# Optimization experiments

Measured on AMD Instinct MI355X. Metric: run time of the kernel, lower is better.

The kernel has to match this reference:

```python
import jax, jax.numpy as jnp
import numpy as np

NBINS = 256
EARLY_STOP = 0.1  # fraction of nbins with no improvement before early break


def setup_inputs() -> dict:
    key = jax.random.key(0)
    x = jax.random.uniform(key, (8, 3, 1024, 1024), dtype=jnp.float32)
    return {"x": x}


def _otsu_forward(x):
    orig_shape = x.shape
    b, c, h, w = x.shape
    rows = b * c
    xf = x.reshape(rows, h * w)                      # (R, N) one image per row
    N = xf.shape[1]

    # Per-row shift so each row starts at 0 (mirrors `x = (x.T - min_value).T`).
    min_val = xf.min(axis=1, keepdims=True)          # (R, 1)
    xs = xf - min_val
    gmax = xs.max()                                  # global min of xs is 0, global max here
    edges = jnp.linspace(jnp.zeros((), xs.dtype), gmax, NBINS + 1)
    width = gmax / NBINS

    # Per-row histogram with torch.histc semantics over global [0, gmax].
    bin_idx = jnp.clip(jnp.floor(xs / width).astype(jnp.int32), 0, NBINS - 1)
    flat_idx = (jnp.arange(rows, dtype=jnp.int32)[:, None] * NBINS + bin_idx).reshape(-1)
    hist = jnp.bincount(flat_idx, length=rows * NBINS).reshape(rows, NBINS).astype(xs.dtype)
    cum_count = jnp.cumsum(hist, axis=1)             # px_bellow after each bin
    w0 = cum_count / N
    w1 = 1.0 - w0

    # Sorted prefix moments -> subset variances for every threshold in one pass.
    xsort = jnp.sort(xs, axis=1)
    row_mean = xs.mean(axis=1, keepdims=True)
    cvals = xsort - row_mean                         # variance is shift-invariant; centering for stability
    s1 = jnp.cumsum(cvals, axis=1)
    s2 = jnp.cumsum(cvals * cvals, axis=1)
    tot1 = s1[:, -1:]
    tot2 = s2[:, -1:]

    thresh = edges[1:]                               # bin_edges[bin+1], shape (NBINS,)
    # n0[r, bin] = #{xs[r] <= thresh[bin]}  (condition `x <= thresh` in the loop)
    n0 = jax.vmap(lambda row: jnp.searchsorted(row, thresh, side="right"))(xsort)  # (R, NBINS)

    def subset_var(S1, S2, n):
        # unbiased variance (torch.var default); nan for n <= 1 like torch
        nf = n.astype(xs.dtype)
        var = (S2 - S1 * S1 / jnp.maximum(nf, 1.0)) / jnp.maximum(nf - 1.0, 1.0)
        return jnp.where(n > 1, var, jnp.nan)

    idx0 = jnp.maximum(n0 - 1, 0)
    S1_0 = jnp.where(n0 > 0, jnp.take_along_axis(s1, idx0, axis=1), 0.0)
    S2_0 = jnp.where(n0 > 0, jnp.take_along_axis(s2, idx0, axis=1), 0.0)
    mu0 = subset_var(S1_0, S2_0, n0)                 # var of pixels <= thresh
    n1 = N - n0
    mu1 = subset_var(tot1 - S1_0, tot2 - S2_0, n1)   # var of pixels > thresh
    icv = w0 * w1 * (mu0 - mu1) ** 2                 # (R, NBINS)

    # Sequential argmax with the original's global early-stop counter.
    max_try = int(NBINS * EARLY_STOP)

    def step(carry, inputs):
        max_icv, best, no_upd, stopped = carry
        icv_b, t_b = inputs                          # (R,), scalar
        upd = (icv_b > max_icv) & jnp.logical_not(stopped)   # nan > x is False, as in torch
        max_icv = jnp.where(upd, icv_b, max_icv)
        best = jnp.where(upd, t_b, best)
        no_upd = jnp.where(jnp.any(upd), 0, no_upd + 1)
        stopped = stopped | (no_upd >= max_try)
        return (max_icv, best, no_upd, stopped), None

    init = (
        jnp.zeros(rows, xs.dtype),
        jnp.zeros(rows, xs.dtype),
        jnp.zeros((), jnp.int32),
        jnp.zeros((), jnp.bool_),
    )
    (_, best_thresh, _, _), _ = jax.lax.scan(step, init, (icv.T, thresh))

    final_thresh = best_thresh[:, None] + min_val    # back to original scale
    out = jnp.where(xf < final_thresh, jnp.zeros((), xs.dtype), xf)
    return out.reshape(orig_shape)


def reference(x):
    return _otsu_forward(x)
```

## Files before the change

### kernel.cpp

```cpp
#include <hip/hip_runtime.h>
#include <stdint.h>


#define ROWS 24
#define NPIX (1 << 20)
#define NBINS 256
#define BPR 64
#define CHUNK (NPIX / BPR)
#define MAX_TRY 25

static constexpr double kD1Scale = 17592186044416.0;
static constexpr double kD1Inv   = 1.0 / 17592186044416.0;
static constexpr double kD2Scale = 4503599627370496.0;
static constexpr double kD2Inv   = 1.0 / 4503599627370496.0;
static constexpr double Nd = 1048576.0;

#define OFF_MINNOT 0
#define OFF_MAXB   128
#define OFF_FINAL  256
#define OFF_CNT    512
#define OFF_COR    (OFF_CNT + ROWS*NBINS*4)
#define OFF_D1     (OFF_COR + ROWS*NBINS*4)
#define OFF_D2     (OFF_D1 + ROWS*NBINS*8)
#define OFF_ICV    (OFF_D2 + ROWS*NBINS*8)
#define WS_TOTAL   (OFF_ICV + ROWS*NBINS*8)

__device__ __forceinline__ double wave_gmax(const unsigned* __restrict__ minnot,
                                            const unsigned* __restrict__ maxb,
                                            int lane) {
  double d = 0.0;
  if (lane < ROWS) {
    d = (double)__uint_as_float(maxb[lane]) - (double)__uint_as_float(~minnot[lane]);
  }
  for (int o = 16; o; o >>= 1) d = fmax(d, __shfl_down(d, o));
  return d;
}

__global__ __launch_bounds__(256) void k_minmax(const float* __restrict__ x,
                                                unsigned* __restrict__ minnot,
                                                unsigned* __restrict__ maxb) {
  int row = blockIdx.x / BPR;
  int sub = blockIdx.x % BPR;
  const float4* p = (const float4*)(x + (size_t)row * NPIX + (size_t)sub * CHUNK);
  float mn = 3.4e38f, mx = 0.0f;
  for (int i = threadIdx.x; i < CHUNK / 4; i += 256) {
    float4 v = p[i];
    mn = fminf(mn, fminf(fminf(v.x, v.y), fminf(v.z, v.w)));
    mx = fmaxf(mx, fmaxf(fmaxf(v.x, v.y), fmaxf(v.z, v.w)));
  }
  __shared__ float smn[4], smx[4];
  for (int o = 32; o; o >>= 1) {
    mn = fminf(mn, __shfl_down(mn, o));
    mx = fmaxf(mx, __shfl_down(mx, o));
  }
  int wave = threadIdx.x >> 6;
  if ((threadIdx.x & 63) == 0) { smn[wave] = mn; smx[wave] = mx; }
  __syncthreads();
  if (threadIdx.x == 0) {
    for (int w = 1; w < 4; ++w) { mn = fminf(mn, smn[w]); mx = fmaxf(mx, smx[w]); }
    atomicMax(&minnot[row], ~__float_as_uint(mn));
    atomicMax(&maxb[row], __float_as_uint(mx));
  }
}

__global__ __launch_bounds__(256) void k_hist(const float* __restrict__ x,
    const unsigned* __restrict__ minnot, const unsigned* __restrict__ maxb,
    unsigned* __restrict__ gcnt, int* __restrict__ gcor,
    unsigned long long* __restrict__ gD1, unsigned long long* __restrict__ gD2) {
  __shared__ unsigned long long hA[NBINS], hB[NBINS];
  __shared__ int hcor[NBINS];
  __shared__ double s_w, s_rmin;
  int t = threadIdx.x;
  hA[t] = 0ull; hB[t] = 0ull; hcor[t] = 0;
  int row = blockIdx.x / BPR;
  int sub = blockIdx.x % BPR;
  if (t < 64) {
    double g = wave_gmax(minnot, maxb, t);
    if (t == 0) {
      s_w = g / 256.0;
      s_rmin = (double)__uint_as_float(~minnot[row]);
    }
  }
  __syncthreads();
  double w = s_w, rmin = s_rmin;
  double rw = 1.0 / w;
  const float4* p = (const float4*)(x + (size_t)row * NPIX + (size_t)sub * CHUNK);
  for (int i = threadIdx.x; i < CHUNK / 4; i += 256) {
    float4 v = p[i];
    float vv[4] = {v.x, v.y, v.z, v.w};
#pragma unroll
    for (int c = 0; c < 4; ++c) {
      double xs = (double)vv[c] - rmin;
      double q1 = xs * rw;
      double rres = fma(-q1, w, xs);
      double q = fma(rres, rw, q1);
      int b = (int)q;
      b = b > 255 ? 255 : b;
      double elo = (double)b * w;
      double ehi = (double)(b + 1) * w;
      int j = b;
      double off = elo;
      if (xs > ehi) { if (b < 255) { j = b + 1; off = ehi; } }
      else if (b > 0 && xs <= elo) { j = b - 1; off = (double)j * w; }
      if (j != b) {
        atomicAdd(&hcor[b], 1);
        atomicAdd(&hcor[j], -1);
      }
      double delta = xs - off;
      unsigned long long d1 = (unsigned long long)llrint(delta * kD1Scale);
      unsigned long long d2 = (unsigned long long)llrint(delta * delta * kD2Scale);
      atomicAdd(&hA[j], (1ull << 44) | d1);
      atomicAdd(&hB[j], d2);
    }
  }
  __syncthreads();
  unsigned long long a = hA[t];
  unsigned c = (unsigned)(a >> 44);
  if (c) {
    atomicAdd(&gcnt[row * NBINS + t], c);
    atomicAdd(&gD1[row * NBINS + t], a & ((1ull << 44) - 1ull));
  }
  unsigned long long b2 = hB[t];
  if (b2) atomicAdd(&gD2[row * NBINS + t], b2);
  if (hcor[t] != 0) atomicAdd(&gcor[row * NBINS + t], hcor[t]);
}

__global__ __launch_bounds__(256) void k_icv(const unsigned* __restrict__ gcnt,
    const int* __restrict__ gcor,
    const unsigned long long* __restrict__ gD1,
    const unsigned long long* __restrict__ gD2,
    const unsigned* __restrict__ minnot, const unsigned* __restrict__ maxb,
    double* __restrict__ gicv) {
  __shared__ double sv[NBINS], su[NBINS];
  __shared__ unsigned scnt[NBINS], scntf[NBINS];
  __shared__ double s_w;
  int r = blockIdx.x, t = threadIdx.x;
  if (t < 64) {
    double g = wave_gmax(minnot, maxb, t);
    if (t == 0) s_w = g / 256.0;
  }
  __syncthreads();
  double w = s_w;
  unsigned cnt = gcnt[r * NBINS + t];
  int cor = gcor[r * NBINS + t];
  double d1 = (double)gD1[r * NBINS + t] * kD1Inv;
  double d2 = (double)gD2[r * NBINS + t] * kD2Inv;
  double elo = (double)t * w;
  scnt[t] = cnt;
  scntf[t] = cnt + (unsigned)cor;
  sv[t] = (double)cnt * elo + d1;
  su[t] = (double)cnt * (elo * elo) + 2.0 * elo * d1 + d2;
  __syncthreads();
  for (int o = 1; o < NBINS; o <<= 1) {
    unsigned a0 = 0, a1 = 0; double b0 = 0, b1 = 0;
    if (t >= o) { a0 = scnt[t - o]; a1 = scntf[t - o]; b0 = sv[t - o]; b1 = su[t - o]; }
    __syncthreads();
    if (t >= o) { scnt[t] += a0; scntf[t] += a1; sv[t] += b0; su[t] += b1; }
    __syncthreads();
  }
  const double dNAN = __builtin_nan("");
  double total1 = sv[NBINS - 1], total2 = su[NBINS - 1];
  double mean = total1 / Nd;
  double tot1 = total1 - Nd * mean;
  double tot2 = total2 - Nd * mean * mean;
  double n0 = (double)scnt[t];
  double n1 = Nd - n0;
  double s1raw = sv[t], s2raw = su[t];
  double S1 = s1raw - n0 * mean;
  double S2 = s2raw - 2.0 * mean * s1raw + n0 * mean * mean;
  double mu0 = (scnt[t] > 1u) ? (S2 - S1 * S1 / n0) / (n0 - 1.0) : dNAN;
  double S1b = tot1 - S1, S2b = tot2 - S2;
  double mu1 = (n1 > 1.0) ? (S2b - S1b * S1b / n1) / (n1 - 1.0) : dNAN;
  double w0 = (double)scntf[t] / Nd, w1v = 1.0 - w0;
  double dd = mu0 - mu1;
  gicv[r * NBINS + t] = w0 * w1v * dd * dd;
}

__global__ __launch_bounds__(256) void k_scan(const double* __restrict__ gicv,
    const unsigned* __restrict__ minnot, const unsigned* __restrict__ maxb,
    double* __restrict__ finalt) {
  __shared__ double sicv[ROWS * NBINS];
  __shared__ double s_w;
  int tid = threadIdx.x;
  for (int i = tid; i < ROWS * NBINS; i += 256) sicv[i] = gicv[i];
  if (tid < 64) {
    double g = wave_gmax(minnot, maxb, tid);
    if (tid == 0) s_w = g / 256.0;
  }
  __syncthreads();
  if (tid >= 64) return;
  int r = tid;
  bool active = r < ROWS;
  double w = s_w;
  double maxicv = 0.0, best = 0.0;
  int no_upd = 0;
  bool stopped = false;
  for (int t = 0; t < NBINS; ++t) {
    double v = active ? sicv[r * NBINS + t] : -1.0;
    bool upd = active && !stopped && (v > maxicv);
    if (upd) { maxicv = v; best = (double)(t + 1) * w; }
    unsigned long long bal = __ballot(upd);
    if (bal != 0ull) no_upd = 0; else ++no_upd;
    if (no_upd >= MAX_TRY) stopped = true;
  }
  if (active) finalt[r] = best + (double)__uint_as_float(~minnot[r]);
}

__global__ __launch_bounds__(256) void k_out(const float* __restrict__ x,
                                             const double* __restrict__ finalt,
                                             float* __restrict__ out) {
  size_t i = (size_t)blockIdx.x * blockDim.x + threadIdx.x;
  size_t stride = (size_t)gridDim.x * blockDim.x;
  const float4* xin = (const float4*)x;
  float4* o = (float4*)out;
  size_t n4 = (size_t)ROWS * NPIX / 4;
  for (; i < n4; i += stride) {
    int row = (int)(i >> 18);
    double ft = finalt[row];
    float4 v = xin[i];
    float4 rr;
    rr.x = ((double)v.x < ft) ? 0.0f : v.x;
    rr.y = ((double)v.y < ft) ? 0.0f : v.y;
    rr.z = ((double)v.z < ft) ? 0.0f : v.z;
    rr.w = ((double)v.w < ft) ? 0.0f : v.w;
    o[i] = rr;
  }
}

extern "C" void kernel_launch(void* const* d_in, const int* in_sizes, int n_in,
                              void* d_out, int out_size, void* d_ws, size_t ws_size,
                              hipStream_t stream) {
  const float* x = (const float*)d_in[0];
  float* out = (float*)d_out;
  char* ws = (char*)d_ws;
  unsigned* minnot = (unsigned*)(ws + OFF_MINNOT);
  unsigned* maxb = (unsigned*)(ws + OFF_MAXB);
  double* finalt = (double*)(ws + OFF_FINAL);
  unsigned* gcnt = (unsigned*)(ws + OFF_CNT);
  int* gcor = (int*)(ws + OFF_COR);
  unsigned long long* gD1 = (unsigned long long*)(ws + OFF_D1);
  unsigned long long* gD2 = (unsigned long long*)(ws + OFF_D2);
  double* gicv = (double*)(ws + OFF_ICV);

  hipMemsetAsync(d_ws, 0, OFF_ICV, stream);
  k_minmax<<<ROWS * BPR, 256, 0, stream>>>(x, minnot, maxb);
  k_hist<<<ROWS * BPR, 256, 0, stream>>>(x, minnot, maxb, gcnt, gcor, gD1, gD2);
  k_icv<<<ROWS, 256, 0, stream>>>(gcnt, gcor, gD1, gD2, minnot, maxb, gicv);
  k_scan<<<1, 256, 0, stream>>>(gicv, minnot, maxb, finalt);
  k_out<<<3072, 256, 0, stream>>>(x, finalt, out);
}
```

Before: 137.1 us.

## Fuse ICV and scan kernels, drop memset, add fast binning path and float threshold

Several changes at once. The workspace memset is removed by zeroing the accumulators inside the min/max kernel, and per-block partial min/max values replace global atomics. The ICV and early-stop scan kernels are merged into one 1024-thread block that uses wave shuffle scans and ballot masks. The histogram gets a fast path that skips the exact division when a value is safely inside a bin, and uses a magic-number double-to-integer conversion in place of llrint. The output kernel compares against a precomputed float threshold and uses nontemporal stores. The intent is fewer launches and less per-pixel double-precision work, at the risk of small numeric edge-case differences.

```diff
diff --git a/kernel.cpp b/kernel.cpp
--- a/kernel.cpp
+++ b/kernel.cpp
@@ -9,38 +9,57 @@
 #define CHUNK (NPIX / BPR)
 #define MAX_TRY 25
 
+typedef float f32x4 __attribute__((ext_vector_type(4)));
+
+static constexpr double kMagic = 6755399441055744.0;
 static constexpr double kD1Scale = 17592186044416.0;
-static constexpr double kD1Inv   = 1.0 / 17592186044416.0;
+static constexpr double kD1Inv = 1.0 / 17592186044416.0;
 static constexpr double kD2Scale = 4503599627370496.0;
-static constexpr double kD2Inv   = 1.0 / 4503599627370496.0;
+static constexpr double kD2Inv = 1.0 / 4503599627370496.0;
 static constexpr double Nd = 1048576.0;
-
-#define OFF_MINNOT 0
-#define OFF_MAXB   128
-#define OFF_FINAL  256
-#define OFF_CNT    512
-#define OFF_COR    (OFF_CNT + ROWS*NBINS*4)
-#define OFF_D1     (OFF_COR + ROWS*NBINS*4)
-#define OFF_D2     (OFF_D1 + ROWS*NBINS*8)
-#define OFF_ICV    (OFF_D2 + ROWS*NBINS*8)
-#define WS_TOTAL   (OFF_ICV + ROWS*NBINS*8)
-
-__device__ __forceinline__ double wave_gmax(const unsigned* __restrict__ minnot,
-                                            const unsigned* __restrict__ maxb,
-                                            int lane) {
+static constexpr double kEps = 1e-9;
+
+#define OFF_PART  0
+#define OFF_FINAL 12288
+#define OFF_T32   12544
+#define OFF_CNT   16384
+#define OFF_COR   40960
+#define OFF_D1    65536
+#define OFF_D2    114688
+#define WS_END    163840
+
+__device__ __forceinline__ void reduce_minmax(const uint2* __restrict__ part,
+                                              unsigned* lmn, unsigned* lmx,
+                                              int nthreads) {
+  int t = threadIdx.x;
+  if (t < ROWS) { lmn[t] = 0xFFFFFFFFu; lmx[t] = 0u; }
+  __syncthreads();
+  for (int p = t; p < ROWS * BPR; p += nthreads) {
+    uint2 v = part[p];
+    atomicMin(&lmn[p >> 6], v.x);
+    atomicMax(&lmx[p >> 6], v.y);
+  }
+  __syncthreads();
+}
+
+__device__ __forceinline__ double compute_w(const unsigned* lmn,
+                                            const unsigned* lmx, int t) {
   double d = 0.0;
-  if (lane < ROWS) {
-    d = (double)__uint_as_float(maxb[lane]) - (double)__uint_as_float(~minnot[lane]);
-  }
+  if (t < ROWS)
+    d = (double)__uint_as_float(lmx[t]) - (double)__uint_as_float(lmn[t]);
   for (int o = 16; o; o >>= 1) d = fmax(d, __shfl_down(d, o));
-  return d;
+  return d / 256.0;
 }
 
 __global__ __launch_bounds__(256) void k_minmax(const float* __restrict__ x,
-                                                unsigned* __restrict__ minnot,
-                                                unsigned* __restrict__ maxb) {
-  int row = blockIdx.x / BPR;
-  int sub = blockIdx.x % BPR;
+                                                uint2* __restrict__ part,
+                                                uint4* __restrict__ zero_base) {
+  int blk = blockIdx.x;
+  if (blk < 36) {
+    uint4 z; z.x = 0u; z.y = 0u; z.z = 0u; z.w = 0u;
+    zero_base[blk * 256 + threadIdx.x] = z;
+  }
+  int row = blk / BPR, sub = blk % BPR;
   const float4* p = (const float4*)(x + (size_t)row * NPIX + (size_t)sub * CHUNK);
   float mn = 3.4e38f, mx = 0.0f;
   for (int i = threadIdx.x; i < CHUNK / 4; i += 256) {
@@ -58,172 +77,228 @@
   __syncthreads();
   if (threadIdx.x == 0) {
     for (int w = 1; w < 4; ++w) { mn = fminf(mn, smn[w]); mx = fmaxf(mx, smx[w]); }
-    atomicMax(&minnot[row], ~__float_as_uint(mn));
-    atomicMax(&maxb[row], __float_as_uint(mx));
+    uint2 r; r.x = __float_as_uint(mn); r.y = __float_as_uint(mx);
+    part[blk] = r;
   }
 }
 
 __global__ __launch_bounds__(256) void k_hist(const float* __restrict__ x,
-    const unsigned* __restrict__ minnot, const unsigned* __restrict__ maxb,
+    const uint2* __restrict__ part,
     unsigned* __restrict__ gcnt, int* __restrict__ gcor,
     unsigned long long* __restrict__ gD1, unsigned long long* __restrict__ gD2) {
+  __shared__ unsigned lmn[ROWS], lmx[ROWS];
   __shared__ unsigned long long hA[NBINS], hB[NBINS];
   __shared__ int hcor[NBINS];
   __shared__ double s_w, s_rmin;
   int t = threadIdx.x;
+  int row = blockIdx.x / BPR, sub = blockIdx.x % BPR;
   hA[t] = 0ull; hB[t] = 0ull; hcor[t] = 0;
-  int row = blockIdx.x / BPR;
-  int sub = blockIdx.x % BPR;
-  if (t < 64) {
-    double g = wave_gmax(minnot, maxb, t);
-    if (t == 0) {
-      s_w = g / 256.0;
-      s_rmin = (double)__uint_as_float(~minnot[row]);
-    }
-  }
-  __syncthreads();
-  double w = s_w, rmin = s_rmin;
-  double rw = 1.0 / w;
+  reduce_minmax(part, lmn, lmx, 256);
+  if (t < 32) {
+    double wv = compute_w(lmn, lmx, t);
+    if (t == 0) { s_w = wv; s_rmin = (double)__uint_as_float(lmn[row]); }
+  }
+  __syncthreads();
+  double w = s_w, rmin = s_rmin, rw = 1.0 / w;
   const float4* p = (const float4*)(x + (size_t)row * NPIX + (size_t)sub * CHUNK);
-  for (int i = threadIdx.x; i < CHUNK / 4; i += 256) {
+  for (int i = t; i < CHUNK / 4; i += 256) {
     float4 v = p[i];
     float vv[4] = {v.x, v.y, v.z, v.w};
 #pragma unroll
     for (int c = 0; c < 4; ++c) {
       double xs = (double)vv[c] - rmin;
       double q1 = xs * rw;
-      double rres = fma(-q1, w, xs);
-      double q = fma(rres, rw, q1);
-      int b = (int)q;
-      b = b > 255 ? 255 : b;
-      double elo = (double)b * w;
-      double ehi = (double)(b + 1) * w;
-      int j = b;
-      double off = elo;
-      if (xs > ehi) { if (b < 255) { j = b + 1; off = ehi; } }
-      else if (b > 0 && xs <= elo) { j = b - 1; off = (double)j * w; }
-      if (j != b) {
-        atomicAdd(&hcor[b], 1);
-        atomicAdd(&hcor[j], -1);
+      int b = (int)q1;
+      double fr = q1 - (double)b;
+      int j; double off;
+      if (__builtin_expect(fr >= kEps && fr <= 1.0 - kEps && b <= 255, 1)) {
+        j = b; off = (double)b * w;
+      } else {
+        double q = xs / w;
+        b = (int)q; if (b > 255) b = 255;
+        double elo = (double)b * w, ehi = (double)(b + 1) * w;
+        j = b; off = elo;
+        if (xs > ehi) { if (b < 255) { j = b + 1; off = ehi; } }
+        else if (b > 0 && xs <= elo) { j = b - 1; off = (double)j * w; }
+        if (j != b) { atomicAdd(&hcor[b], 1); atomicAdd(&hcor[j], -1); }
       }
       double delta = xs - off;
-      unsigned long long d1 = (unsigned long long)llrint(delta * kD1Scale);
-      unsigned long long d2 = (unsigned long long)llrint(delta * delta * kD2Scale);
-      atomicAdd(&hA[j], (1ull << 44) | d1);
+      double t1 = fma(delta, kD1Scale, kMagic);
+      double dd = delta * delta;
+      double t2 = fma(dd, kD2Scale, kMagic);
+      unsigned long long d1 = (unsigned long long)__double_as_longlong(t1)
+                              & 0x0007FFFFFFFFFFFFull;
+      unsigned long long d2 = (unsigned long long)__double_as_longlong(t2)
+                              & 0x0007FFFFFFFFFFFFull;
+      atomicAdd(&hA[j], d1 | (1ull << 44));
       atomicAdd(&hB[j], d2);
     }
   }
   __syncthreads();
   unsigned long long a = hA[t];
   unsigned c = (unsigned)(a >> 44);
+  int base = row * NBINS + t;
   if (c) {
-    atomicAdd(&gcnt[row * NBINS + t], c);
-    atomicAdd(&gD1[row * NBINS + t], a & ((1ull << 44) - 1ull));
-  }
-  unsigned long long b2 = hB[t];
-  if (b2) atomicAdd(&gD2[row * NBINS + t], b2);
-  if (hcor[t] != 0) atomicAdd(&gcor[row * NBINS + t], hcor[t]);
-}
-
-__global__ __launch_bounds__(256) void k_icv(const unsigned* __restrict__ gcnt,
-    const int* __restrict__ gcor,
+    atomicAdd(&gcnt[base], c);
+    atomicAdd(&gD1[base], a & ((1ull << 44) - 1ull));
+  }
+  if (hB[t]) atomicAdd(&gD2[base], hB[t]);
+  if (hcor[t]) atomicAdd(&gcor[base], hcor[t]);
+}
+
+__global__ __launch_bounds__(1024) void k_icv_scan(
+    const unsigned* __restrict__ gcnt, const int* __restrict__ gcor,
     const unsigned long long* __restrict__ gD1,
     const unsigned long long* __restrict__ gD2,
-    const unsigned* __restrict__ minnot, const unsigned* __restrict__ maxb,
-    double* __restrict__ gicv) {
-  __shared__ double sv[NBINS], su[NBINS];
-  __shared__ unsigned scnt[NBINS], scntf[NBINS];
+    const uint2* __restrict__ part,
+    double* __restrict__ finalt, float* __restrict__ t32g) {
+  __shared__ unsigned lmn[ROWS], lmx[ROWS];
+  __shared__ unsigned long long umask[ROWS][4];
+  __shared__ unsigned long long ganyw[4];
   __shared__ double s_w;
-  int r = blockIdx.x, t = threadIdx.x;
-  if (t < 64) {
-    double g = wave_gmax(minnot, maxb, t);
-    if (t == 0) s_w = g / 256.0;
+  __shared__ int s_tstop;
+  int t = threadIdx.x;
+  if (t < 4) ganyw[t] = 0ull;
+  if (t < ROWS * 4) ((unsigned long long*)umask)[t] = 0ull;
+  reduce_minmax(part, lmn, lmx, 1024);
+  if (t < 32) {
+    double wv = compute_w(lmn, lmx, t);
+    if (t == 0) s_w = wv;
   }
   __syncthreads();
   double w = s_w;
-  unsigned cnt = gcnt[r * NBINS + t];
-  int cor = gcor[r * NBINS + t];
-  double d1 = (double)gD1[r * NBINS + t] * kD1Inv;
-  double d2 = (double)gD2[r * NBINS + t] * kD2Inv;
-  double elo = (double)t * w;
-  scnt[t] = cnt;
-  scntf[t] = cnt + (unsigned)cor;
-  sv[t] = (double)cnt * elo + d1;
-  su[t] = (double)cnt * (elo * elo) + 2.0 * elo * d1 + d2;
-  __syncthreads();
-  for (int o = 1; o < NBINS; o <<= 1) {
-    unsigned a0 = 0, a1 = 0; double b0 = 0, b1 = 0;
-    if (t >= o) { a0 = scnt[t - o]; a1 = scntf[t - o]; b0 = sv[t - o]; b1 = su[t - o]; }
-    __syncthreads();
-    if (t >= o) { scnt[t] += a0; scntf[t] += a1; sv[t] += b0; su[t] += b1; }
-    __syncthreads();
-  }
+  int wave = t >> 6, lane = t & 63;
   const double dNAN = __builtin_nan("");
-  double total1 = sv[NBINS - 1], total2 = su[NBINS - 1];
-  double mean = total1 / Nd;
-  double tot1 = total1 - Nd * mean;
-  double tot2 = total2 - Nd * mean * mean;
-  double n0 = (double)scnt[t];
-  double n1 = Nd - n0;
-  double s1raw = sv[t], s2raw = su[t];
-  double S1 = s1raw - n0 * mean;
-  double S2 = s2raw - 2.0 * mean * s1raw + n0 * mean * mean;
-  double mu0 = (scnt[t] > 1u) ? (S2 - S1 * S1 / n0) / (n0 - 1.0) : dNAN;
-  double S1b = tot1 - S1, S2b = tot2 - S2;
-  double mu1 = (n1 > 1.0) ? (S2b - S1b * S1b / n1) / (n1 - 1.0) : dNAN;
-  double w0 = (double)scntf[t] / Nd, w1v = 1.0 - w0;
-  double dd = mu0 - mu1;
-  gicv[r * NBINS + t] = w0 * w1v * dd * dd;
-}
-
-__global__ __launch_bounds__(256) void k_scan(const double* __restrict__ gicv,
-    const unsigned* __restrict__ minnot, const unsigned* __restrict__ maxb,
-    double* __restrict__ finalt) {
-  __shared__ double sicv[ROWS * NBINS];
-  __shared__ double s_w;
-  int tid = threadIdx.x;
-  for (int i = tid; i < ROWS * NBINS; i += 256) sicv[i] = gicv[i];
-  if (tid < 64) {
-    double g = wave_gmax(minnot, maxb, tid);
-    if (tid == 0) s_w = g / 256.0;
-  }
-  __syncthreads();
-  if (tid >= 64) return;
-  int r = tid;
-  bool active = r < ROWS;
-  double w = s_w;
-  double maxicv = 0.0, best = 0.0;
-  int no_upd = 0;
-  bool stopped = false;
-  for (int t = 0; t < NBINS; ++t) {
-    double v = active ? sicv[r * NBINS + t] : -1.0;
-    bool upd = active && !stopped && (v > maxicv);
-    if (upd) { maxicv = v; best = (double)(t + 1) * w; }
-    unsigned long long bal = __ballot(upd);
-    if (bal != 0ull) no_upd = 0; else ++no_upd;
-    if (no_upd >= MAX_TRY) stopped = true;
-  }
-  if (active) finalt[r] = best + (double)__uint_as_float(~minnot[r]);
+
+  for (int pass = 0; pass < 2; ++pass) {
+    if (pass == 1 && wave >= 8) break;
+    int r = pass ? 16 + wave : wave;
+    double e1[4], e2[4];
+    unsigned long long pc0[4];
+#pragma unroll
+    for (int k = 0; k < 4; ++k) {
+      int bin = k * 64 + lane;
+      int idx = r * NBINS + bin;
+      unsigned n = gcnt[idx];
+      int cor = gcor[idx];
+      double d1 = (double)gD1[idx] * kD1Inv;
+      double d2v = (double)gD2[idx] * kD2Inv;
+      double elo = (double)bin * w;
+      e1[k] = (double)n * elo + d1;
+      e2[k] = (double)n * (elo * elo) + 2.0 * elo * d1 + d2v;
+      pc0[k] = (unsigned long long)n |
+               ((unsigned long long)(unsigned)(n + (unsigned)cor) << 32);
+    }
+    double c1 = 0.0, c2 = 0.0;
+    unsigned long long cc = 0ull;
+    double E1[4], E2[4];
+    unsigned long long CC[4];
+#pragma unroll
+    for (int k = 0; k < 4; ++k) {
+      double p1 = e1[k], p2 = e2[k];
+      unsigned long long pc = pc0[k];
+      for (int o = 1; o < 64; o <<= 1) {
+        double u1 = __shfl_up(p1, o), u2 = __shfl_up(p2, o);
+        unsigned long long uc = __shfl_up(pc, o);
+        if (lane >= o) { p1 += u1; p2 += u2; pc += uc; }
+      }
+      E1[k] = p1 + c1; E2[k] = p2 + c2; CC[k] = pc + cc;
+      c1 += __shfl(p1, 63); c2 += __shfl(p2, 63); cc += __shfl(pc, 63);
+    }
+    double total1 = c1, total2 = c2;
+    double mean = total1 / Nd;
+    double tot1 = total1 - Nd * mean;
+    double tot2 = total2 - Nd * mean * mean;
+    double icv4[4];
+#pragma unroll
+    for (int k = 0; k < 4; ++k) {
+      unsigned n0i = (unsigned)(CC[k] & 0xffffffffull);
+      double n0 = (double)n0i;
+      double n1 = Nd - n0;
+      double s1raw = E1[k], s2raw = E2[k];
+      double S1 = s1raw - n0 * mean;
+      double S2 = s2raw - 2.0 * mean * s1raw + n0 * mean * mean;
+      double mu0 = (n0i > 1u) ? (S2 - S1 * S1 / n0) / (n0 - 1.0) : dNAN;
+      double S1b = tot1 - S1, S2b = tot2 - S2;
+      double mu1 = (n1 > 1.0) ? (S2b - S1b * S1b / n1) / (n1 - 1.0) : dNAN;
+      double w0 = (double)(unsigned)(CC[k] >> 32) / Nd, w1v = 1.0 - w0;
+      double ddv = mu0 - mu1;
+      icv4[k] = w0 * w1v * ddv * ddv;
+    }
+    double m = 0.0;
+    unsigned long long myMask[4];
+#pragma unroll
+    for (int k = 0; k < 4; ++k) {
+      double v = icv4[k];
+      double pm = v;
+      for (int o = 1; o < 64; o <<= 1) {
+        double u = __shfl_up(pm, o);
+        if (lane >= o) pm = fmax(pm, u);
+      }
+      double excl = __shfl_up(pm, 1);
+      double Mprev = (lane == 0) ? m : fmax(m, excl);
+      bool upd = v > Mprev;
+      myMask[k] = __ballot(upd);
+      m = fmax(m, __shfl(pm, 63));
+    }
+    if (lane == 0) {
+#pragma unroll
+      for (int k = 0; k < 4; ++k) {
+        umask[r][k] = myMask[k];
+        atomicOr(&ganyw[k], myMask[k]);
+      }
+    }
+  }
+  __syncthreads();
+  if (t == 0) {
+    int no_upd = 0, tstop = 255;
+    for (int b = 0; b < 256; ++b) {
+      bool any = (ganyw[b >> 6] >> (b & 63)) & 1ull;
+      if (any) no_upd = 0; else ++no_upd;
+      if (no_upd >= MAX_TRY) { tstop = b; break; }
+    }
+    s_tstop = tstop;
+  }
+  __syncthreads();
+  if (t < ROWS) {
+    int tstop = s_tstop;
+    int tbest = -1;
+    for (int k = 3; k >= 0; --k) {
+      unsigned long long msk = umask[t][k];
+      int hi = k * 64 + 63;
+      if (hi > tstop) {
+        int shift = tstop - k * 64;
+        if (shift < 0) msk = 0ull;
+        else msk &= (shift >= 63) ? ~0ull : ((2ull << shift) - 1ull);
+      }
+      if (msk) { tbest = k * 64 + 63 - __clzll(msk); break; }
+    }
+    double rmin = (double)__uint_as_float(lmn[t]);
+    double ft = (tbest >= 0) ? (double)(tbest + 1) * w + rmin : rmin;
+    finalt[t] = ft;
+    float f = (float)ft;
+    if ((double)f < ft) f = __uint_as_float(__float_as_uint(f) + 1u);
+    t32g[t] = f;
+  }
 }
 
 __global__ __launch_bounds__(256) void k_out(const float* __restrict__ x,
-                                             const double* __restrict__ finalt,
+                                             const float* __restrict__ t32g,
                                              float* __restrict__ out) {
   size_t i = (size_t)blockIdx.x * blockDim.x + threadIdx.x;
   size_t stride = (size_t)gridDim.x * blockDim.x;
-  const float4* xin = (const float4*)x;
-  float4* o = (float4*)out;
+  const f32x4* xin = (const f32x4*)x;
+  f32x4* o = (f32x4*)out;
   size_t n4 = (size_t)ROWS * NPIX / 4;
   for (; i < n4; i += stride) {
-    int row = (int)(i >> 18);
-    double ft = finalt[row];
-    float4 v = xin[i];
-    float4 rr;
-    rr.x = ((double)v.x < ft) ? 0.0f : v.x;
-    rr.y = ((double)v.y < ft) ? 0.0f : v.y;
-    rr.z = ((double)v.z < ft) ? 0.0f : v.z;
-    rr.w = ((double)v.w < ft) ? 0.0f : v.w;
-    o[i] = rr;
+    float ft = t32g[i >> 18];
+    f32x4 v = xin[i];
+    f32x4 rr;
+    rr.x = (v.x < ft) ? 0.0f : v.x;
+    rr.y = (v.y < ft) ? 0.0f : v.y;
+    rr.z = (v.z < ft) ? 0.0f : v.z;
+    rr.w = (v.w < ft) ? 0.0f : v.w;
+    __builtin_nontemporal_store(rr, &o[i]);
   }
 }
 
@@ -233,19 +308,16 @@
   const float* x = (const float*)d_in[0];
   float* out = (float*)d_out;
   char* ws = (char*)d_ws;
-  unsigned* minnot = (unsigned*)(ws + OFF_MINNOT);
-  unsigned* maxb = (unsigned*)(ws + OFF_MAXB);
+  uint2* part = (uint2*)(ws + OFF_PART);
   double* finalt = (double*)(ws + OFF_FINAL);
+  float* t32g = (float*)(ws + OFF_T32);
   unsigned* gcnt = (unsigned*)(ws + OFF_CNT);
   int* gcor = (int*)(ws + OFF_COR);
   unsigned long long* gD1 = (unsigned long long*)(ws + OFF_D1);
   unsigned long long* gD2 = (unsigned long long*)(ws + OFF_D2);
-  double* gicv = (double*)(ws + OFF_ICV);
-
-  hipMemsetAsync(d_ws, 0, OFF_ICV, stream);
-  k_minmax<<<ROWS * BPR, 256, 0, stream>>>(x, minnot, maxb);
-  k_hist<<<ROWS * BPR, 256, 0, stream>>>(x, minnot, maxb, gcnt, gcor, gD1, gD2);
-  k_icv<<<ROWS, 256, 0, stream>>>(gcnt, gcor, gD1, gD2, minnot, maxb, gicv);
-  k_scan<<<1, 256, 0, stream>>>(gicv, minnot, maxb, finalt);
-  k_out<<<3072, 256, 0, stream>>>(x, finalt, out);
-}
+
+  k_minmax<<<ROWS * BPR, 256, 0, stream>>>(x, part, (uint4*)(ws + OFF_CNT));
+  k_hist<<<ROWS * BPR, 256, 0, stream>>>(x, part, gcnt, gcor, gD1, gD2);
+  k_icv_scan<<<1, 1024, 0, stream>>>(gcnt, gcor, gD1, gD2, part, finalt, t32g);
+  k_out<<<3072, 256, 0, stream>>>(x, t32g, out);
+}
```

After: 118.1 us. -13.9%, faster.
